# Kernel tuning notes

Measured on AMD Instinct MI355X. Metric: run time of the kernel, lower is better.

Reference implementation:

```python
import jax, jax.numpy as jnp
import numpy as np

N = 20000      # num_nodes
H = 150        # hidden_channels
R = 35         # num_relations
B = 5          # num_blocks  -> block dims 30x30
E = 640000     # num_edges
IB = H // B


def _xavier(key, shape):
    fan_in, fan_out = shape[-2], shape[-1]
    lim = jnp.sqrt(6.0 / (fan_in + fan_out))
    return jax.random.uniform(key, shape, jnp.float32, -lim, lim)


def setup_inputs() -> dict:
    key = jax.random.key(0)
    ks = jax.random.split(key, 10)
    edge_index = jax.random.randint(ks[0], (2, E), 0, N, dtype=jnp.int64)
    edge_type = jax.random.randint(ks[1], (E,), 0, R, dtype=jnp.int64)
    return {
        "node_emb": _xavier(ks[2], (N, H)),
        "w1": _xavier(ks[3], (R, B, IB, IB)),      # relation block-diagonal weights
        "root1": _xavier(ks[4], (H, H)),
        "b1": jnp.zeros((H,), jnp.float32),
        "w2": _xavier(ks[5], (R, B, IB, IB)),
        "root2": _xavier(ks[6], (H, H)),
        "b2": jnp.zeros((H,), jnp.float32),
        "edge_index": edge_index,
        "edge_type": edge_type,
    }


def _rgcn_layer(x, w, root, bias, src, dst, etype):
    # PyG RGCNConv with num_blocks: per-relation block-diag transform of source
    # features, mean-aggregated per (dst, relation), summed over relations,
    # plus dense root transform and bias.
    # Linearity lets us aggregate (mean) FIRST, then transform: cheaper + exact.
    seg = dst * R + etype                                   # [E] segment per (node, rel)
    xs = x[src]                                             # [E, H] gather
    sums = jax.ops.segment_sum(xs, seg, num_segments=N * R)  # [N*R, H]
    cnt = jax.ops.segment_sum(jnp.ones((src.shape[0],), x.dtype), seg,
                              num_segments=N * R)           # [N*R]
    mean = sums / jnp.maximum(cnt, 1.0)[:, None]            # zero where no edges
    a = mean.reshape(N, R, B, IB)
    agg = jnp.einsum('nrbi,rbio->nbo', a, w).reshape(N, H)  # sum over relations
    return agg + x @ root + bias


def reference(node_emb, w1, root1, b1, w2, root2, b2, edge_index, edge_type):
    src, dst = edge_index[0], edge_index[1]
    x = _rgcn_layer(node_emb, w1, root1, b1, src, dst, edge_type)
    x = jax.nn.relu(x)
    # dropout p=0.2 is a no-op in eval mode
    x = _rgcn_layer(x, w2, root2, b2, src, dst, edge_type)
    return x
```

## Files before the change

### kernel.cpp

```cpp
#include <hip/hip_runtime.h>
#include <hip/hip_fp16.h>

#define H 150
#define RNUM 35
#define BNUM 5
#define IB 30

typedef unsigned short ushort_t;
typedef unsigned int uint_t;
using bf16x8 = __attribute__((ext_vector_type(8))) short;
using f32x4  = __attribute__((ext_vector_type(4))) float;

__device__ __forceinline__ ushort_t f2bf(float x) {
    union { float f; unsigned u; } v; v.f = x;
    unsigned u = v.u;
    return (ushort_t)((u + 0x7FFF + ((u >> 16) & 1)) >> 16);
}


__global__ void k_count(const int* __restrict__ ei, const int* __restrict__ et,
                        int E_, int* __restrict__ cnt) {
    for (int e = blockIdx.x * blockDim.x + threadIdx.x; e < E_; e += gridDim.x * blockDim.x) {
        int d = ei[E_ + e];
        int r = et[e];
        atomicAdd(&cnt[d * RNUM + r], 1);
    }
}

#define SPT 2
#define SCAN_BLOCK 256
#define SCAN_SPAN (SPT * SCAN_BLOCK)

__global__ void k_scanA(const int* __restrict__ cnt, int N_,
                        int* __restrict__ blkN, int* __restrict__ blkD) {
    __shared__ int sn[SCAN_BLOCK], sd[SCAN_BLOCK];
    int t = threadIdx.x;
    int base = blockIdx.x * SCAN_SPAN + t * SPT;
    int tn = 0, td = 0;
    for (int k = 0; k < SPT; ++k) {
        int d = base + k;
        if (d < N_) {
            for (int r = 0; r < RNUM; ++r) {
                int c = cnt[d * RNUM + r];
                if (c) { tn++; td += c; }
            }
        }
    }
    sn[t] = tn; sd[t] = td;
    __syncthreads();
    if (t == 0) {
        int an = 0, ad = 0;
        for (int i = 0; i < SCAN_BLOCK; ++i) { an += sn[i]; ad += sd[i]; }
        blkN[blockIdx.x] = an; blkD[blockIdx.x] = ad;
    }
}

__global__ void k_scanB(const int* __restrict__ blkN, const int* __restrict__ blkD,
                        int* __restrict__ blkBN, int* __restrict__ blkBD, int nblk) {
    if (threadIdx.x == 0 && blockIdx.x == 0) {
        int an = 0, ad = 0;
        for (int i = 0; i < nblk; ++i) {
            blkBN[i] = an; blkBD[i] = ad;
            an += blkN[i]; ad += blkD[i];
        }
    }
}

__global__ void k_scanC(const int* __restrict__ cnt, int N_,
                        const int* __restrict__ blkBN, const int* __restrict__ blkBD,
                        int* __restrict__ dstbase, int* __restrict__ segoff,
                        int* __restrict__ segidx, int* __restrict__ relhist2) {
    __shared__ int sn[SCAN_BLOCK], sd[SCAN_BLOCK];
    __shared__ int lhist[RNUM];
    int t = threadIdx.x;
    for (int i = t; i < RNUM; i += SCAN_BLOCK) lhist[i] = 0;
    int base = blockIdx.x * SCAN_SPAN + t * SPT;
    int tn = 0, td = 0;
    for (int k = 0; k < SPT; ++k) {
        int d = base + k;
        if (d < N_) {
            for (int r = 0; r < RNUM; ++r) {
                int c = cnt[d * RNUM + r];
                if (c) { tn++; td += c; }
            }
        }
    }
    sn[t] = tn; sd[t] = td;
    __syncthreads();
    if (t == 0) {
        int an = blkBN[blockIdx.x], ad = blkBD[blockIdx.x];
        for (int i = 0; i < SCAN_BLOCK; ++i) {
            int a = sn[i], b = sd[i];
            sn[i] = an; sd[i] = ad;
            an += a; ad += b;
        }
    }
    __syncthreads();
    int sb = sn[t], eb = sd[t];
    for (int k = 0; k < SPT; ++k) {
        int d = base + k;
        if (d < N_) {
            dstbase[d] = sb;
            for (int r = 0; r < RNUM; ++r) {
                int cell = d * RNUM + r;
                int c = cnt[cell];
                segoff[cell] = eb;
                if (c) { segidx[cell] = sb; sb++; eb += c; atomicAdd(&lhist[r], 1); }
            }
            if (d == N_ - 1) dstbase[N_] = sb;
        }
    }
    __syncthreads();
    for (int i = t; i < RNUM; i += SCAN_BLOCK)
        if (lhist[i]) atomicAdd(&relhist2[i], lhist[i]);
}

__global__ void k_relbase(const int* __restrict__ relhist2, int* __restrict__ relbase2) {
    if (threadIdx.x == 0 && blockIdx.x == 0) {
        int a = 0;
        for (int r = 0; r < RNUM; ++r) { relbase2[r] = a; a += relhist2[r]; }
        relbase2[RNUM] = a;
    }
}

__global__ void k_scatter2(const int* __restrict__ ei, const int* __restrict__ et,
                           int E_, int* __restrict__ segoff, int* __restrict__ ssrc2) {
    int e = blockIdx.x * blockDim.x + threadIdx.x;
    if (e >= E_) return;
    int r = et[e];
    int d = ei[E_ + e];
    int pos = atomicAdd(&segoff[d * RNUM + r], 1);
    ssrc2[pos] = ei[e];
}

__global__ void k_relassign(const int* __restrict__ cnt, const int* __restrict__ segoff,
                            const int* __restrict__ segidx, int Ncells,
                            const int* __restrict__ relbase2, int* __restrict__ relfill2,
                            int4* __restrict__ rec) {
    __shared__ int lh[RNUM];
    __shared__ int lbase[RNUM];
    for (int i = threadIdx.x; i < RNUM; i += blockDim.x) lh[i] = 0;
    __syncthreads();
    const int stride = gridDim.x * blockDim.x;
    for (int cell = blockIdx.x * blockDim.x + threadIdx.x; cell < Ncells; cell += stride)
        if (cnt[cell]) atomicAdd(&lh[cell % RNUM], 1);
    __syncthreads();
    for (int i = threadIdx.x; i < RNUM; i += blockDim.x) {
        int c = lh[i];
        lbase[i] = relbase2[i] + (c ? atomicAdd(&relfill2[i], c) : 0);
        lh[i] = 0;
    }
    __syncthreads();
    for (int cell = blockIdx.x * blockDim.x + threadIdx.x; cell < Ncells; cell += stride) {
        int c = cnt[cell];
        if (c) {
            int r = cell % RNUM;
            int pos = lbase[r] + atomicAdd(&lh[r], 1);
            rec[pos] = make_int4(segidx[cell], segoff[cell] - c, c, 0);
        }
    }
}

__global__ void k_prepw(const float* __restrict__ w1, const float* __restrict__ w2,
                        ushort_t* __restrict__ wb1, ushort_t* __restrict__ wb2) {
    const int tot = RNUM * BNUM * 2 * 16 * 32;
    int idx = blockIdx.x * blockDim.x + threadIdx.x;
    if (idx >= 2 * tot) return;
    const float* w = (idx < tot) ? w1 : w2;
    ushort_t* wb = (idx < tot) ? wb1 : wb2;
    int q = (idx < tot) ? idx : idx - tot;
    int kj = q & 7;
    int kg = (q >> 3) & 3;
    int cl = (q >> 5) & 15;
    int nh = (q >> 9) & 1;
    int rb = q >> 10;
    int k = kg * 8 + kj;
    int col = nh * 16 + cl;
    ushort_t v = 0;
    if (k < IB && col < IB) v = f2bf(w[(rb * IB + k) * IB + col]);
    wb[q] = v;
}

__global__ void k_convA(const float* __restrict__ x, ushort_t* __restrict__ Abf, int N_) {
    int i = blockIdx.x * blockDim.x + threadIdx.x;
    if (i >= N_ * 160) return;
    int n = i / 160, c = i - n * 160;
    Abf[i] = (c < H) ? f2bf(x[n * H + c]) : 0;
}

__global__ void k_convB(const float* __restrict__ r1, const float* __restrict__ r2,
                        ushort_t* __restrict__ B1, ushort_t* __restrict__ B2) {
    int i = blockIdx.x * blockDim.x + threadIdx.x;
    if (i >= 2 * 160 * 160) return;
    const float* src = (i < 160 * 160) ? r1 : r2;
    ushort_t* dst = (i < 160 * 160) ? B1 : B2;
    int k = (i < 160 * 160) ? i : i - 160 * 160;
    int row = k / 160, col = k - row * 160;
    dst[k] = (row < H && col < H) ? f2bf(src[row * H + col]) : 0;
}

__global__ __launch_bounds__(256) void k_rootmm(const ushort_t* __restrict__ Abf,
                                                const ushort_t* __restrict__ Bbf,
                                                const float* __restrict__ bias,
                                                float* __restrict__ Cout, int N_) {
    int nt = blockIdx.y;
    int wv = threadIdx.x >> 6, l = threadIdx.x & 63;
    int lr = l & 15, lk = l >> 4;
    bf16x8 bfr[5];
    #pragma unroll
    for (int ks = 0; ks < 5; ++ks) {
        #pragma unroll
        for (int j = 0; j < 8; ++j)
            bfr[ks][j] = (short)Bbf[(ks * 32 + lk * 8 + j) * 160 + nt * 16 + lr];
    }
    int mtiles = N_ / 16;
    int col = nt * 16 + lr;
    float bv = (col < H) ? bias[col] : 0.f;
    for (int mt = blockIdx.x * 4 + wv; mt < mtiles; mt += gridDim.x * 4) {
        f32x4 acc = {0.f, 0.f, 0.f, 0.f};
        const ushort_t* arow = Abf + (size_t)(mt * 16 + lr) * 160 + lk * 8;
        #pragma unroll
        for (int ks = 0; ks < 5; ++ks) {
            bf16x8 af = *reinterpret_cast<const bf16x8*>(arow + ks * 32);
            acc = __builtin_amdgcn_mfma_f32_16x16x32_bf16(af, bfr[ks], acc, 0, 0, 0);
        }
        if (col < H) {
            #pragma unroll
            for (int reg = 0; reg < 4; ++reg)
                Cout[(size_t)(mt * 16 + lk * 4 + reg) * H + col] = acc[reg] + bv;
        }
    }
}


#define ASTRIDE 168

__global__ __launch_bounds__(256, 4)
void k_seg(const int4* __restrict__ rec, const int* __restrict__ relbase2,
           const int* __restrict__ ssrc2, const ushort_t* __restrict__ wbf,
           const float* __restrict__ xin, __half* __restrict__ tseg,
           const int* __restrict__ rowLoP, const int* __restrict__ rowHiP) {
    __shared__ ushort_t Abuf[4][16 * ASTRIDE];
    int rowLo = rowLoP[0], rowHi = rowHiP[0];
    int r = blockIdx.y;
    int base = relbase2[r];
    int nseg = relbase2[r + 1] - base;
    int t = threadIdx.x, wv = t >> 6, l = t & 63;
    int lr = l & 15, kg = l >> 4;

    bf16x8 bfr[BNUM][2];
    #pragma unroll
    for (int b = 0; b < BNUM; ++b)
        #pragma unroll
        for (int nh = 0; nh < 2; ++nh)
            bfr[b][nh] = *reinterpret_cast<const bf16x8*>(
                wbf + ((size_t)((r * BNUM + b) * 2 + nh) * 512) + lr * 32 + kg * 8);

    {
        uint_t* az = reinterpret_cast<uint_t*>(&Abuf[wv][0]);
        for (int i = l; i < 16 * ASTRIDE / 2; i += 64) az[i] = 0;
    }

    int o0 = (l / 30) * 32 + (l % 30);
    int o1 = ((l + 64) / 30) * 32 + ((l + 64) % 30);
    int o2 = ((l + 128) / 30) * 32 + ((l + 128) % 30);

    int ntile = (nseg + 15) >> 4;
    for (int ti = blockIdx.x * 4 + wv; ti < ntile; ti += gridDim.x * 4) {
        int sbeg = ti << 4;
        int4 myrec = make_int4(0x7fffffff, 0, 0, 0);
        if (l < 16 && sbeg + l < nseg) myrec = rec[base + sbeg + l];

        for (int s = 0; s < 16; ++s) {
            int row = __builtin_amdgcn_readfirstlane(__shfl(myrec.x, s));
            if (row < rowLo || row >= rowHi) continue;
            int eo = __builtin_amdgcn_readfirstlane(__shfl(myrec.y, s));
            int c  = __builtin_amdgcn_readfirstlane(__shfl(myrec.z, s));
            float a0 = 0.f, a1 = 0.f, a2 = 0.f;
            for (int k = 0; k < c; ++k) {
                int src = ssrc2[eo + k];
                const float* xr = xin + (size_t)src * H;
                a0 += xr[l];
                a1 += xr[l + 64];
                if (l < 22) a2 += xr[l + 128];
            }
            float inv = 1.0f / (float)c;
            ushort_t* Aw = &Abuf[wv][s * ASTRIDE];
            Aw[o0] = f2bf(a0 * inv);
            Aw[o1] = f2bf(a1 * inv);
            if (l < 22) Aw[o2] = f2bf(a2 * inv);
        }

        int rg[4]; bool rok[4];
        #pragma unroll
        for (int q = 0; q < 4; ++q) {
            rg[q] = __shfl(myrec.x, kg * 4 + q);
            rok[q] = (rg[q] >= rowLo) && (rg[q] < rowHi);
        }

        #pragma unroll
        for (int b = 0; b < BNUM; ++b) {
            bf16x8 af = *reinterpret_cast<const bf16x8*>(
                &Abuf[wv][lr * ASTRIDE + b * 32 + kg * 8]);
            f32x4 acc0 = {0.f, 0.f, 0.f, 0.f};
            f32x4 acc1 = {0.f, 0.f, 0.f, 0.f};
            acc0 = __builtin_amdgcn_mfma_f32_16x16x32_bf16(af, bfr[b][0], acc0, 0, 0, 0);
            acc1 = __builtin_amdgcn_mfma_f32_16x16x32_bf16(af, bfr[b][1], acc1, 0, 0, 0);
            #pragma unroll
            for (int q = 0; q < 4; ++q) {
                if (rok[q]) {
                    __half* orow = tseg + (size_t)(rg[q] - rowLo) * H + b * IB;
                    orow[lr] = __float2half(acc0[q]);
                    if (lr < 14) orow[16 + lr] = __float2half(acc1[q]);
                }
            }
        }
    }
}

__global__ __launch_bounds__(256)
void k_aggadd(const __half* __restrict__ tseg, const int* __restrict__ dstbase,
              float* __restrict__ buf, ushort_t* __restrict__ Abf,
              int relu, int s0, int s1) {
    int t = threadIdx.x, wv = t >> 6, l = t & 63;
    int segBase = dstbase[s0];
    for (int d = s0 + blockIdx.x * 4 + wv; d < s1; d += gridDim.x * 4) {
        int a = dstbase[d], bnd = dstbase[d + 1];
        float* brow = buf + (size_t)d * H;
        float2 acc0 = *reinterpret_cast<const float2*>(brow + 2 * l);
        float2 acc1 = make_float2(0.f, 0.f);
        if (l < 11) acc1 = *reinterpret_cast<const float2*>(brow + 128 + 2 * l);
        for (int s = a; s < bnd; ++s) {
            const __half2* trow = reinterpret_cast<const __half2*>(
                tseg + (size_t)(s - segBase) * H);
            float2 v = __half22float2(trow[l]);
            acc0.x += v.x; acc0.y += v.y;
            if (l < 11) {
                float2 v1 = __half22float2(trow[64 + l]);
                acc1.x += v1.x; acc1.y += v1.y;
            }
        }
        if (relu) {
            acc0.x = fmaxf(acc0.x, 0.f); acc0.y = fmaxf(acc0.y, 0.f);
            acc1.x = fmaxf(acc1.x, 0.f); acc1.y = fmaxf(acc1.y, 0.f);
        }
        *reinterpret_cast<float2*>(brow + 2 * l) = acc0;
        if (l < 11) *reinterpret_cast<float2*>(brow + 128 + 2 * l) = acc1;
        if (Abf) {
            ushort_t* arow = Abf + (size_t)d * 160;
            uint_t p0 = (uint_t)f2bf(acc0.x) | ((uint_t)f2bf(acc0.y) << 16);
            *reinterpret_cast<uint_t*>(arow + 2 * l) = p0;
            if (l < 11) {
                uint_t p1 = (uint_t)f2bf(acc1.x) | ((uint_t)f2bf(acc1.y) << 16);
                *reinterpret_cast<uint_t*>(arow + 128 + 2 * l) = p1;
            }
            if (l < 5) *reinterpret_cast<uint_t*>(arow + 150 + 2 * l) = 0;
        }
    }
}

extern "C" void kernel_launch(void* const* d_in, const int* in_sizes, int n_in,
                              void* d_out, int out_size, void* d_ws, size_t ws_size,
                              hipStream_t stream) {
    const float* node_emb = (const float*)d_in[0];
    const float* w1 = (const float*)d_in[1];
    const float* root1 = (const float*)d_in[2];
    const float* b1 = (const float*)d_in[3];
    const float* w2 = (const float*)d_in[4];
    const float* root2 = (const float*)d_in[5];
    const float* b2 = (const float*)d_in[6];
    const int* edge_index = (const int*)d_in[7];
    const int* edge_type = (const int*)d_in[8];
    int N_ = in_sizes[0] / H;
    int E_ = in_sizes[8];
    float* out = (float*)d_out;

    const int Ncells = N_ * RNUM;
    const int wbtot = RNUM * BNUM * 2 * 16 * 32;

    int* ws = (int*)d_ws;
    size_t off = 0;
    int* cnt      = ws + off; off += Ncells;
    int* relhist2 = ws + off; off += 64;
    int* relfill2 = ws + off; off += 64;
    size_t zero_units = off;
    int* relbase2 = ws + off; off += 64;
    int* blkN     = ws + off; off += 64;
    int* blkD     = ws + off; off += 64;
    int* blkBN    = ws + off; off += 64;
    int* blkBD    = ws + off; off += 64;
    int* dstbase  = ws + off; off += N_ + 2;
    int* segoff   = ws + off; off += Ncells;
    int* segidx   = ws + off; off += Ncells;
    int* ssrc2    = ws + off; off += E_;
    off = (off + 3) & ~(size_t)3;
    int4* rec     = (int4*)(ws + off); off += (size_t)4 * Ncells;
    ushort_t* wbf1 = (ushort_t*)(ws + off); off += wbtot / 2;
    ushort_t* wbf2 = (ushort_t*)(ws + off); off += wbtot / 2;
    ushort_t* Bbf1 = (ushort_t*)(ws + off); off += 12800;
    ushort_t* Bbf2 = (ushort_t*)(ws + off); off += 12800;
    ushort_t* Abf  = (ushort_t*)(ws + off); off += (size_t)N_ * 160 / 2;
    float* buf1   = (float*)(ws + off); off += (size_t)N_ * H;
    __half* tseg  = (__half*)(ws + off);
    size_t tsegOffB = off * 4;

    size_t availB = (ws_size > tsegOffB) ? (ws_size - tsegOffB) : 0;
    long long dps_ll = (long long)(availB / ((size_t)RNUM * H * 2));
    int dps = (dps_ll > N_) ? N_ : (int)dps_ll;
    if (dps < 1) dps = 1;
    int nstripe = (N_ + dps - 1) / dps;

    hipMemsetAsync(cnt, 0, zero_units * 4, stream);

    k_count<<<512, 256, 0, stream>>>(edge_index, edge_type, E_, cnt);
    int nscan = (N_ + SCAN_SPAN - 1) / SCAN_SPAN;
    k_scanA<<<nscan, SCAN_BLOCK, 0, stream>>>(cnt, N_, blkN, blkD);
    k_scanB<<<1, 64, 0, stream>>>(blkN, blkD, blkBN, blkBD, nscan);
    k_scanC<<<nscan, SCAN_BLOCK, 0, stream>>>(cnt, N_, blkBN, blkBD, dstbase, segoff,
                                              segidx, relhist2);
    k_relbase<<<1, 64, 0, stream>>>(relhist2, relbase2);
    k_scatter2<<<(E_ + 255) / 256, 256, 0, stream>>>(edge_index, edge_type, E_, segoff, ssrc2);
    k_relassign<<<64, 256, 0, stream>>>(cnt, segoff, segidx, Ncells, relbase2, relfill2, rec);
    k_prepw<<<(2 * wbtot + 255) / 256, 256, 0, stream>>>(w1, w2, wbf1, wbf2);
    k_convB<<<(2 * 160 * 160 + 255) / 256, 256, 0, stream>>>(root1, root2, Bbf1, Bbf2);
    k_convA<<<(N_ * 160 + 255) / 256, 256, 0, stream>>>(node_emb, Abf, N_);

    dim3 segGrid(64, RNUM);

    k_rootmm<<<dim3(40, 10), 256, 0, stream>>>(Abf, Bbf1, b1, buf1, N_);
    for (int st = 0; st < nstripe; ++st) {
        int s0 = st * dps;
        int s1 = s0 + dps; if (s1 > N_) s1 = N_;
        k_seg<<<segGrid, 256, 0, stream>>>(rec, relbase2, ssrc2, wbf1, node_emb, tseg,
                                           dstbase + s0, dstbase + s1);
        k_aggadd<<<1280, 256, 0, stream>>>(tseg, dstbase, buf1, Abf, 1, s0, s1);
    }

    k_rootmm<<<dim3(40, 10), 256, 0, stream>>>(Abf, Bbf2, b2, out, N_);
    for (int st = 0; st < nstripe; ++st) {
        int s0 = st * dps;
        int s1 = s0 + dps; if (s1 > N_) s1 = N_;
        k_seg<<<segGrid, 256, 0, stream>>>(rec, relbase2, ssrc2, wbf2, buf1, tseg,
                                           dstbase + s0, dstbase + s1);
        k_aggadd<<<1280, 256, 0, stream>>>(tseg, dstbase, out, (ushort_t*)nullptr, 0, s0, s1);
    }
}
```

Measured before the change: 506.2 us.

## Gather bf16 node features in k_seg and flatten relation tiles into 1D grid

The segment kernel now gathers source rows from a padded bf16 copy of the features (xbf for layer 1, the bf16 post-ReLU Abf for layer 2) instead of fp32. Each lane reads packed 32-bit pairs and writes packed pairs into LDS, which roughly halves gather bandwidth. The 2D grid (64 x relations) becomes a flat 1792-block grid over a prefix of per-relation tile counts, with a binary search to find each tile's relation, which balances work across relations. The trade-off is reduced input precision for the layer-1 gather, plus reloading the weight fragments per tile.

```diff
diff --git a/kernel.cpp b/kernel.cpp
--- a/kernel.cpp
+++ b/kernel.cpp
@@ -15,6 +15,12 @@
     union { float f; unsigned u; } v; v.f = x;
     unsigned u = v.u;
     return (ushort_t)((u + 0x7FFF + ((u >> 16) & 1)) >> 16);
+}
+__device__ __forceinline__ float bfLo(uint_t u) {
+    union { unsigned u; float f; } v; v.u = u << 16; return v.f;
+}
+__device__ __forceinline__ float bfHi(uint_t u) {
+    union { unsigned u; float f; } v; v.u = u & 0xffff0000u; return v.f;
 }
 
 
@@ -115,11 +121,16 @@
         if (lhist[i]) atomicAdd(&relhist2[i], lhist[i]);
 }
 
-__global__ void k_relbase(const int* __restrict__ relhist2, int* __restrict__ relbase2) {
+__global__ void k_relbase(const int* __restrict__ relhist2, int* __restrict__ relbase2,
+                          int* __restrict__ tprefix) {
     if (threadIdx.x == 0 && blockIdx.x == 0) {
-        int a = 0;
-        for (int r = 0; r < RNUM; ++r) { relbase2[r] = a; a += relhist2[r]; }
-        relbase2[RNUM] = a;
+        int a = 0, tp = 0;
+        for (int r = 0; r < RNUM; ++r) {
+            relbase2[r] = a; tprefix[r] = tp;
+            a += relhist2[r];
+            tp += (relhist2[r] + 15) >> 4;
+        }
+        relbase2[RNUM] = a; tprefix[RNUM] = tp;
     }
 }
 
@@ -181,11 +192,11 @@
     wb[q] = v;
 }
 
-__global__ void k_convA(const float* __restrict__ x, ushort_t* __restrict__ Abf, int N_) {
+__global__ void k_convA(const float* __restrict__ x, ushort_t* __restrict__ xbf, int N_) {
     int i = blockIdx.x * blockDim.x + threadIdx.x;
     if (i >= N_ * 160) return;
     int n = i / 160, c = i - n * 160;
-    Abf[i] = (c < H) ? f2bf(x[n * H + c]) : 0;
+    xbf[i] = (c < H) ? f2bf(x[n * H + c]) : 0;
 }
 
 __global__ void k_convB(const float* __restrict__ r1, const float* __restrict__ r2,
@@ -237,58 +248,76 @@
 
 __global__ __launch_bounds__(256, 4)
 void k_seg(const int4* __restrict__ rec, const int* __restrict__ relbase2,
+           const int* __restrict__ tprefix,
            const int* __restrict__ ssrc2, const ushort_t* __restrict__ wbf,
-           const float* __restrict__ xin, __half* __restrict__ tseg,
+           const ushort_t* __restrict__ xbf, __half* __restrict__ tseg,
            const int* __restrict__ rowLoP, const int* __restrict__ rowHiP) {
     __shared__ ushort_t Abuf[4][16 * ASTRIDE];
-    int rowLo = rowLoP[0], rowHi = rowHiP[0];
-    int r = blockIdx.y;
-    int base = relbase2[r];
-    int nseg = relbase2[r + 1] - base;
+    __shared__ int relb[RNUM + 1], tpre[RNUM + 1];
     int t = threadIdx.x, wv = t >> 6, l = t & 63;
     int lr = l & 15, kg = l >> 4;
-
-    bf16x8 bfr[BNUM][2];
-    #pragma unroll
-    for (int b = 0; b < BNUM; ++b)
-        #pragma unroll
-        for (int nh = 0; nh < 2; ++nh)
-            bfr[b][nh] = *reinterpret_cast<const bf16x8*>(
-                wbf + ((size_t)((r * BNUM + b) * 2 + nh) * 512) + lr * 32 + kg * 8);
+    if (t < RNUM + 1) { relb[t] = relbase2[t]; tpre[t] = tprefix[t]; }
+    __syncthreads();
+    int rowLo = rowLoP[0], rowHi = rowHiP[0];
+    int ntile_tot = tpre[RNUM];
 
     {
         uint_t* az = reinterpret_cast<uint_t*>(&Abuf[wv][0]);
         for (int i = l; i < 16 * ASTRIDE / 2; i += 64) az[i] = 0;
     }
 
-    int o0 = (l / 30) * 32 + (l % 30);
-    int o1 = ((l + 64) / 30) * 32 + ((l + 64) % 30);
-    int o2 = ((l + 128) / 30) * 32 + ((l + 128) % 30);
-
-    int ntile = (nseg + 15) >> 4;
-    for (int ti = blockIdx.x * 4 + wv; ti < ntile; ti += gridDim.x * 4) {
-        int sbeg = ti << 4;
-        int4 myrec = make_int4(0x7fffffff, 0, 0, 0);
+    int i0 = 2 * l;
+    int uA = (i0 / 30) * 16 + (i0 % 30) / 2 ? 0 : 0;
+    uA = ((i0 / 30) * 32 + (i0 % 30)) >> 1;
+    int i1 = 128 + 2 * l;
+    int uB = ((i1 / 30) * 32 + (i1 % 30)) >> 1;
+
+    for (int ti = blockIdx.x * 4 + wv; ti < ntile_tot; ti += gridDim.x * 4) {
+        int r_lo = 0, r_hi = RNUM;
+        while (r_hi - r_lo > 1) {
+            int m = (r_lo + r_hi) >> 1;
+            if (tpre[m] <= ti) r_lo = m; else r_hi = m;
+        }
+        int r = r_lo;
+        int base = relb[r];
+        int nseg = relb[r + 1] - base;
+        int sbeg = (ti - tpre[r]) << 4;
+
+        bf16x8 bfr[BNUM][2];
+        #pragma unroll
+        for (int b = 0; b < BNUM; ++b)
+            #pragma unroll
+            for (int nh = 0; nh < 2; ++nh)
+                bfr[b][nh] = *reinterpret_cast<const bf16x8*>(
+                    wbf + ((size_t)((r * BNUM + b) * 2 + nh) * 512) + lr * 32 + kg * 8);
+
+        int4 myrec = make_int4(0x7fffffff, 0, 1, 0);
         if (l < 16 && sbeg + l < nseg) myrec = rec[base + sbeg + l];
 
+        uint_t* Au = reinterpret_cast<uint_t*>(&Abuf[wv][0]);
         for (int s = 0; s < 16; ++s) {
             int row = __builtin_amdgcn_readfirstlane(__shfl(myrec.x, s));
             if (row < rowLo || row >= rowHi) continue;
             int eo = __builtin_amdgcn_readfirstlane(__shfl(myrec.y, s));
             int c  = __builtin_amdgcn_readfirstlane(__shfl(myrec.z, s));
-            float a0 = 0.f, a1 = 0.f, a2 = 0.f;
+            float a0 = 0.f, a1 = 0.f, a2 = 0.f, a3 = 0.f;
             for (int k = 0; k < c; ++k) {
                 int src = ssrc2[eo + k];
-                const float* xr = xin + (size_t)src * H;
-                a0 += xr[l];
-                a1 += xr[l + 64];
-                if (l < 22) a2 += xr[l + 128];
+                const uint_t* rowU = reinterpret_cast<const uint_t*>(xbf + (size_t)src * 160);
+                uint_t u0 = rowU[l];
+                a0 += bfLo(u0); a1 += bfHi(u0);
+                if (l < 11) {
+                    uint_t u1 = rowU[64 + l];
+                    a2 += bfLo(u1); a3 += bfHi(u1);
+                }
             }
             float inv = 1.0f / (float)c;
-            ushort_t* Aw = &Abuf[wv][s * ASTRIDE];
-            Aw[o0] = f2bf(a0 * inv);
-            Aw[o1] = f2bf(a1 * inv);
-            if (l < 22) Aw[o2] = f2bf(a2 * inv);
+            uint_t p0 = (uint_t)f2bf(a0 * inv) | ((uint_t)f2bf(a1 * inv) << 16);
+            Au[s * 84 + uA] = p0;
+            if (l < 11) {
+                uint_t p1 = (uint_t)f2bf(a2 * inv) | ((uint_t)f2bf(a3 * inv) << 16);
+                Au[s * 84 + uB] = p1;
+            }
         }
 
         int rg[4]; bool rok[4];
@@ -318,15 +347,16 @@
     }
 }
 
+
 __global__ __launch_bounds__(256)
 void k_aggadd(const __half* __restrict__ tseg, const int* __restrict__ dstbase,
-              float* __restrict__ buf, ushort_t* __restrict__ Abf,
-              int relu, int s0, int s1) {
+              const float* __restrict__ rootsrc, float* __restrict__ fout,
+              ushort_t* __restrict__ Abf, int relu, int s0, int s1) {
     int t = threadIdx.x, wv = t >> 6, l = t & 63;
     int segBase = dstbase[s0];
     for (int d = s0 + blockIdx.x * 4 + wv; d < s1; d += gridDim.x * 4) {
         int a = dstbase[d], bnd = dstbase[d + 1];
-        float* brow = buf + (size_t)d * H;
+        const float* brow = rootsrc + (size_t)d * H;
         float2 acc0 = *reinterpret_cast<const float2*>(brow + 2 * l);
         float2 acc1 = make_float2(0.f, 0.f);
         if (l < 11) acc1 = *reinterpret_cast<const float2*>(brow + 128 + 2 * l);
@@ -344,8 +374,11 @@
             acc0.x = fmaxf(acc0.x, 0.f); acc0.y = fmaxf(acc0.y, 0.f);
             acc1.x = fmaxf(acc1.x, 0.f); acc1.y = fmaxf(acc1.y, 0.f);
         }
-        *reinterpret_cast<float2*>(brow + 2 * l) = acc0;
-        if (l < 11) *reinterpret_cast<float2*>(brow + 128 + 2 * l) = acc1;
+        if (fout) {
+            float* frow = fout + (size_t)d * H;
+            *reinterpret_cast<float2*>(frow + 2 * l) = acc0;
+            if (l < 11) *reinterpret_cast<float2*>(frow + 128 + 2 * l) = acc1;
+        }
         if (Abf) {
             ushort_t* arow = Abf + (size_t)d * 160;
             uint_t p0 = (uint_t)f2bf(acc0.x) | ((uint_t)f2bf(acc0.y) << 16);
@@ -385,6 +418,7 @@
     int* relfill2 = ws + off; off += 64;
     size_t zero_units = off;
     int* relbase2 = ws + off; off += 64;
+    int* tprefix  = ws + off; off += 64;
     int* blkN     = ws + off; off += 64;
     int* blkD     = ws + off; off += 64;
     int* blkBN    = ws + off; off += 64;
@@ -399,8 +433,9 @@
     ushort_t* wbf2 = (ushort_t*)(ws + off); off += wbtot / 2;
     ushort_t* Bbf1 = (ushort_t*)(ws + off); off += 12800;
     ushort_t* Bbf2 = (ushort_t*)(ws + off); off += 12800;
+    ushort_t* xbf  = (ushort_t*)(ws + off); off += (size_t)N_ * 160 / 2;
     ushort_t* Abf  = (ushort_t*)(ws + off); off += (size_t)N_ * 160 / 2;
-    float* buf1   = (float*)(ws + off); off += (size_t)N_ * H;
+    float* rootbuf = (float*)(ws + off); off += (size_t)N_ * H;
     __half* tseg  = (__half*)(ws + off);
     size_t tsegOffB = off * 4;
 
@@ -418,30 +453,32 @@
     k_scanB<<<1, 64, 0, stream>>>(blkN, blkD, blkBN, blkBD, nscan);
     k_scanC<<<nscan, SCAN_BLOCK, 0, stream>>>(cnt, N_, blkBN, blkBD, dstbase, segoff,
                                               segidx, relhist2);
-    k_relbase<<<1, 64, 0, stream>>>(relhist2, relbase2);
+    k_relbase<<<1, 64, 0, stream>>>(relhist2, relbase2, tprefix);
     k_scatter2<<<(E_ + 255) / 256, 256, 0, stream>>>(edge_index, edge_type, E_, segoff, ssrc2);
     k_relassign<<<64, 256, 0, stream>>>(cnt, segoff, segidx, Ncells, relbase2, relfill2, rec);
     k_prepw<<<(2 * wbtot + 255) / 256, 256, 0, stream>>>(w1, w2, wbf1, wbf2);
     k_convB<<<(2 * 160 * 160 + 255) / 256, 256, 0, stream>>>(root1, root2, Bbf1, Bbf2);
-    k_convA<<<(N_ * 160 + 255) / 256, 256, 0, stream>>>(node_emb, Abf, N_);
-
-    dim3 segGrid(64, RNUM);
-
-    k_rootmm<<<dim3(40, 10), 256, 0, stream>>>(Abf, Bbf1, b1, buf1, N_);
+    k_convA<<<(N_ * 160 + 255) / 256, 256, 0, stream>>>(node_emb, xbf, N_);
+
+    const int SEG_GRID = 1792;
+
+    k_rootmm<<<dim3(40, 10), 256, 0, stream>>>(xbf, Bbf1, b1, rootbuf, N_);
     for (int st = 0; st < nstripe; ++st) {
         int s0 = st * dps;
         int s1 = s0 + dps; if (s1 > N_) s1 = N_;
-        k_seg<<<segGrid, 256, 0, stream>>>(rec, relbase2, ssrc2, wbf1, node_emb, tseg,
-                                           dstbase + s0, dstbase + s1);
-        k_aggadd<<<1280, 256, 0, stream>>>(tseg, dstbase, buf1, Abf, 1, s0, s1);
+        k_seg<<<SEG_GRID, 256, 0, stream>>>(rec, relbase2, tprefix, ssrc2, wbf1, xbf, tseg,
+                                            dstbase + s0, dstbase + s1);
+        k_aggadd<<<1280, 256, 0, stream>>>(tseg, dstbase, rootbuf, (float*)nullptr, Abf,
+                                           1, s0, s1);
     }
 
     k_rootmm<<<dim3(40, 10), 256, 0, stream>>>(Abf, Bbf2, b2, out, N_);
     for (int st = 0; st < nstripe; ++st) {
         int s0 = st * dps;
         int s1 = s0 + dps; if (s1 > N_) s1 = N_;
-        k_seg<<<segGrid, 256, 0, stream>>>(rec, relbase2, ssrc2, wbf2, buf1, tseg,
-                                           dstbase + s0, dstbase + s1);
-        k_aggadd<<<1280, 256, 0, stream>>>(tseg, dstbase, out, (ushort_t*)nullptr, 0, s0, s1);
-    }
-}
+        k_seg<<<SEG_GRID, 256, 0, stream>>>(rec, relbase2, tprefix, ssrc2, wbf2, Abf, tseg,
+                                            dstbase + s0, dstbase + s1);
+        k_aggadd<<<1280, 256, 0, stream>>>(tseg, dstbase, out, out, (ushort_t*)nullptr,
+                                           0, s0, s1);
+    }
+}
```

After: 455.5 us. 1.11x faster.
